# Performance work log

Hardware: AMD Instinct MI355X
Metric: run time of the kernel (lower is better)

## Reference

```python
import jax, jax.numpy as jnp
from jax import lax
import numpy as np

B, IN, HID, OUT, E = 32768, 512, 1024, 2, 64
N_MEM, N_ITER = 100, 10


def setup_inputs() -> dict:
    key = jax.random.key(0)
    ks = jax.random.split(key, 10)
    x = jax.random.normal(ks[0], (B, IN), dtype=jnp.float32)
    # encoder params (Linear stored as [in, out] for x @ W + b)
    e_w1 = jax.random.normal(ks[1], (IN, HID), dtype=jnp.float32) * 0.02
    e_b1 = jnp.zeros((HID,), dtype=jnp.float32)
    e_w2 = jax.random.normal(ks[2], (HID, E), dtype=jnp.float32) * 0.02
    e_b2 = jnp.zeros((E,), dtype=jnp.float32)
    # Hopfield weights: sum of outer products of N_MEM bipolar memories, zero diag, /N_MEM
    mems = jnp.where(jax.random.bernoulli(ks[3], 0.5, (N_MEM, E)), 1.0, -1.0)
    hop_w = (mems.T @ mems) / N_MEM
    hop_w = hop_w * (1.0 - jnp.eye(E, dtype=jnp.float32))
    # Q-network params
    n_w1 = jax.random.normal(ks[4], (IN + E, HID), dtype=jnp.float32) * 0.02
    n_b1 = jnp.zeros((HID,), dtype=jnp.float32)
    n_w2 = jax.random.normal(ks[5], (HID, HID), dtype=jnp.float32) * 0.02
    n_b2 = jnp.zeros((HID,), dtype=jnp.float32)
    n_w3 = jax.random.normal(ks[6], (HID, OUT), dtype=jnp.float32) * 0.02
    n_b3 = jnp.zeros((OUT,), dtype=jnp.float32)
    return {"x": x, "e_w1": e_w1, "e_b1": e_b1, "e_w2": e_w2, "e_b2": e_b2,
            "hop_w": hop_w, "n_w1": n_w1, "n_b1": n_b1, "n_w2": n_w2,
            "n_b2": n_b2, "n_w3": n_w3, "n_b3": n_b3}


def _retrieve(probe, hop_w):
    # Asynchronous Hopfield retrieval, batched over B.
    # probe: [B, E]; state in {+1,-1}
    state = jnp.where(probe > 0, 1.0, -1.0)
    idxs = jnp.arange(E)

    def unit_step(state, xs):
        i, w_row = xs  # w_row: [E]
        act = state @ w_row  # [B]
        state = state.at[:, i].set(jnp.where(act > 0, 1.0, -1.0))
        return state, None

    def iter_body(state, _):
        state, _ = lax.scan(unit_step, state, (idxs, hop_w))
        return state, None

    state, _ = lax.scan(iter_body, state, None, length=N_ITER)
    return jnp.where(state > 0, 1.0, 0.0)


def reference(x, e_w1, e_b1, e_w2, e_b2, hop_w, n_w1, n_b1, n_w2, n_b2, n_w3, n_b3):
    encoded = jax.nn.relu(x @ e_w1 + e_b1) @ e_w2 + e_b2  # [B, E]
    retrieved = lax.stop_gradient(_retrieve(encoded, hop_w))  # detached in original
    combined = jnp.concatenate([x, retrieved], axis=1)  # [B, IN+E]
    h = jax.nn.relu(combined @ n_w1 + n_b1)
    h = jax.nn.relu(h @ n_w2 + n_b2)
    return h @ n_w3 + n_b3  # [B, OUT]
```

## Files before the change

kernel.cpp:

```cpp
#include <hip/hip_runtime.h>
#include <hip/hip_bf16.h>
#include <stdint.h>
#include <math.h>

typedef __attribute__((ext_vector_type(4))) float f32x4;
typedef __attribute__((ext_vector_type(8))) __bf16 bf16x8;
typedef __attribute__((ext_vector_type(8))) uint16_t u16x8;
typedef __attribute__((ext_vector_type(4))) uint32_t u32x4;

__device__ __forceinline__ uint16_t f2bf(float f) {
  union { float f; uint32_t u; } v; v.f = f;
  uint32_t r = v.u + 0x7FFFu + ((v.u >> 16) & 1u);
  return (uint16_t)(r >> 16);
}
__device__ __forceinline__ float bf2f(uint16_t b) {
  union { uint32_t u; float f; } v; v.u = ((uint32_t)b) << 16;
  return v.f;
}
__device__ __forceinline__ void gload16(const void* g, void* l) {
  __builtin_amdgcn_global_load_lds(
      (const __attribute__((address_space(1))) uint32_t*)g,
      (__attribute__((address_space(3))) uint32_t*)l, 16, 0, 0);
}

__global__ __launch_bounds__(256) void k_conv_x(const float* __restrict__ x,
                                                uint16_t* __restrict__ comb) {
  int i = blockIdx.x * 256 + threadIdx.x;
  int base = i * 8;
  int row = base >> 9;
  int col = base & 511;
  const float* src = x + base;
  f32x4 a = *(const f32x4*)src;
  f32x4 b = *(const f32x4*)(src + 4);
  u16x8 o;
  o[0] = f2bf(a[0]); o[1] = f2bf(a[1]); o[2] = f2bf(a[2]); o[3] = f2bf(a[3]);
  o[4] = f2bf(b[0]); o[5] = f2bf(b[1]); o[6] = f2bf(b[2]); o[7] = f2bf(b[3]);
  *(u16x8*)(comb + (size_t)row * 576 + col) = o;
}

__global__ __launch_bounds__(256) void k_convT(const float* __restrict__ W,
                                               uint16_t* __restrict__ WT,
                                               int K, int N) {
  __shared__ float tile[64][65];
  const int t = threadIdx.x;
  const int n0 = blockIdx.x * 64, k0 = blockIdx.y * 64;
  const int c = t & 63, r0 = t >> 6;
#pragma unroll
  for (int rr = 0; rr < 16; ++rr) {
    int r = r0 * 16 + rr;
    tile[r][c] = W[(size_t)(k0 + r) * N + n0 + c];
  }
  __syncthreads();
#pragma unroll
  for (int rr = 0; rr < 16; ++rr) {
    int r = r0 * 16 + rr;
    WT[(size_t)(n0 + r) * K + k0 + c] = f2bf(tile[c][r]);
  }
}

__global__ __launch_bounds__(256) void k_conv(const float* __restrict__ W,
                                              uint16_t* __restrict__ O, int n) {
  int i = blockIdx.x * 256 + threadIdx.x;
  if (i < n) O[i] = f2bf(W[i]);
}

template <int K, bool RELU>
__global__ __launch_bounds__(256, 4)
void k_enc(const float* __restrict__ A, const float* __restrict__ W,
           const float* __restrict__ bias, float* __restrict__ C, int N) {
  __shared__ __align__(16) float xs[32][128];
  __shared__ __align__(16) float ws[32][68];
  const int t = threadIdx.x;
  const int m0 = blockIdx.y * 128, n0 = blockIdx.x * 64;
  const int mg = t >> 4, ng = t & 15;

  float res[8][4], acc[8][4];
#pragma unroll
  for (int i = 0; i < 8; ++i)
#pragma unroll
    for (int j = 0; j < 4; ++j) { res[i][j] = 0.f; acc[i][j] = 0.f; }

  const int xr = t >> 1, xk = (t & 1) * 16;
  const int wrr = t >> 3, wj = (t & 7) * 8;

  for (int c = 0; c < K / 32; ++c) {
    const int k0 = c * 32;
    if (k0 > 0 && (k0 % 384) == 0) {
#pragma unroll
      for (int i = 0; i < 8; ++i)
#pragma unroll
        for (int j = 0; j < 4; ++j) { res[i][j] += acc[i][j]; acc[i][j] = 0.f; }
    }
    __syncthreads();
#pragma unroll
    for (int u = 0; u < 4; ++u) {
      f32x4 v = *(const f32x4*)(A + (size_t)(m0 + xr) * K + k0 + xk + u * 4);
      xs[xk + u * 4 + 0][xr] = v[0];
      xs[xk + u * 4 + 1][xr] = v[1];
      xs[xk + u * 4 + 2][xr] = v[2];
      xs[xk + u * 4 + 3][xr] = v[3];
    }
#pragma unroll
    for (int u = 0; u < 2; ++u)
      *(f32x4*)&ws[wrr][wj + u * 4] =
          *(const f32x4*)(W + (size_t)(k0 + wrr) * N + n0 + wj + u * 4);
    __syncthreads();
#pragma unroll
    for (int k = 0; k < 32; ++k) {
      f32x4 x0 = *(const f32x4*)&xs[k][mg * 8];
      f32x4 x1 = *(const f32x4*)&xs[k][mg * 8 + 4];
      f32x4 wv = *(const f32x4*)&ws[k][ng * 4];
#pragma unroll
      for (int j = 0; j < 4; ++j) {
        acc[0][j] = fmaf(x0[0], wv[j], acc[0][j]);
        acc[1][j] = fmaf(x0[1], wv[j], acc[1][j]);
        acc[2][j] = fmaf(x0[2], wv[j], acc[2][j]);
        acc[3][j] = fmaf(x0[3], wv[j], acc[3][j]);
        acc[4][j] = fmaf(x1[0], wv[j], acc[4][j]);
        acc[5][j] = fmaf(x1[1], wv[j], acc[5][j]);
        acc[6][j] = fmaf(x1[2], wv[j], acc[6][j]);
        acc[7][j] = fmaf(x1[3], wv[j], acc[7][j]);
      }
    }
  }
#pragma unroll
  for (int i = 0; i < 8; ++i)
#pragma unroll
    for (int j = 0; j < 4; ++j) res[i][j] += acc[i][j];

#pragma unroll
  for (int i = 0; i < 8; ++i) {
    f32x4 o;
#pragma unroll
    for (int j = 0; j < 4; ++j) {
      float v = res[i][j] + bias[n0 + ng * 4 + j];
      if (RELU) v = fmaxf(v, 0.f);
      o[j] = v;
    }
    *(f32x4*)(C + (size_t)(m0 + mg * 8 + i) * N + n0 + ng * 4) = o;
  }
}

#define KNIFE_TAU 1e-6f

__device__ __forceinline__ uint32_t retrieve_bits(uint32_t sm,
                                                  const float (*w)[64],
                                                  int l) {
  for (int it = 0; it < 10; ++it) {
    bool changed = false;
    for (int i = 0; i < 64; ++i) {
      float r = 0.f;
#pragma unroll
      for (int c = 0; c < 8; ++c) {
        float wv = w[i][8 * c + l];
        uint32_t flip = ((~sm >> c) & 1u) << 31;
        r += __uint_as_float(__float_as_uint(wv) ^ flip);
      }
      r += __shfl_xor(r, 1);
      r += __shfl_xor(r, 2);
      r += __shfl_xor(r, 4);
      uint32_t nb = r > 0.f ? 1u : 0u;
      if ((i & 7) == l) {
        uint32_t g = i >> 3;
        uint32_t ob = (sm >> g) & 1u;
        changed |= (nb != ob);
        sm = (sm & ~(1u << g)) | (nb << g);
      }
    }
    if (!__any(changed)) break;
  }
  return sm;
}

__device__ __forceinline__ uint64_t gather_mask_bits(uint32_t sm, int g) {
  uint64_t m = 0;
#pragma unroll
  for (int c = 0; c < 8; ++c) {
    unsigned long long b = __ballot(((sm >> c) & 1u) != 0u);
    m |= (uint64_t)((b >> (g * 8)) & 0xFFull) << (8 * c);
  }
  return m;
}

__global__ __launch_bounds__(256) void k_hopfield(const float* __restrict__ enc,
                                                  const float* __restrict__ hw,
                                                  uint16_t* __restrict__ comb) {
  __shared__ __align__(16) float w[64][64];
  const int t = threadIdx.x;
#pragma unroll
  for (int i = 0; i < 4; ++i)
    ((f32x4*)&w[0][0])[t * 4 + i] = ((const f32x4*)hw)[t * 4 + i];
  __syncthreads();

  const int lane = t & 63, wv = t >> 6;
  const int g = lane >> 3, l = lane & 7;
  const int sid = (blockIdx.x * 4 + wv) * 8 + g;
  const float* er = enc + (size_t)sid * 64;

  uint32_t imask = 0;
  int kc = -1;
  bool kpos = false;
#pragma unroll
  for (int c = 0; c < 8; ++c) {
    float v = er[8 * c + l];
    if (v > 0.f) imask |= (1u << c);
    if (kc < 0 && fabsf(v) < KNIFE_TAU) { kc = c; kpos = v > 0.f; }
  }
  unsigned long long kb = __ballot(kc >= 0);
  uint32_t gbits = (uint32_t)((kb >> (g * 8)) & 0xFFull);
  bool hasknife = gbits != 0;
  int klane = g * 8 + (__ffs(gbits) - 1);
  bool is_kl = hasknife && (lane == klane);
  uint32_t kbit = (kc >= 0) ? (1u << (kc & 7)) : 0u;

  uint32_t ma_bits = is_kl ? (imask | kbit) : imask;
  uint64_t mA = gather_mask_bits(retrieve_bits(ma_bits, w, l), g);
  uint64_t m = mA;

  if (__any(hasknife)) {
    if (hasknife) {
      uint32_t mb_bits = is_kl ? (imask & ~kbit) : imask;
      uint64_t mB = gather_mask_bits(retrieve_bits(mb_bits, w, l), g);
      if (mA != mB) {
        int kp = __shfl(kpos ? 1 : 0, klane);
        m = kp ? mA : mB;
      }
    }
  }

  uint32_t byte = (uint32_t)((m >> (8 * l)) & 0xFFull);
  u32x4 o;
#pragma unroll
  for (int p = 0; p < 4; ++p) {
    uint32_t lo = ((byte >> (2 * p)) & 1u) ? 0x3F80u : 0u;
    uint32_t hi = ((byte >> (2 * p + 1)) & 1u) ? 0x3F800000u : 0u;
    o[p] = lo | hi;
  }
  *(u32x4*)(comb + (size_t)sid * 576 + 512 + l * 8) = o;
}

__global__ __launch_bounds__(256)
void k_gemm_bf16(const uint16_t* __restrict__ A, const uint16_t* __restrict__ BT,
                 const float* __restrict__ bias, uint16_t* __restrict__ C,
                 int M, int N, int K, int relu) {
  constexpr int BM = 128, BN = 128, BK = 32;
  __shared__ __align__(16) uint16_t As[BM][BK];
  __shared__ __align__(16) uint16_t Bs[BN][BK];
  const int t = threadIdx.x;
  const int lane = t & 63, wid = t >> 6;
  const int wr = wid >> 1, wc = wid & 1;
  const int bm = blockIdx.y * BM, bn = blockIdx.x * BN;

  f32x4 acc[4][4] = {};

  const int l15 = lane & 15, kb = (lane >> 4) * 8;
  const int i0 = t, i1 = t + 256;
  const int r0 = i0 >> 2, c0 = (i0 & 3) * 8;
  const int r1 = i1 >> 2, c1 = (i1 & 3) * 8;
  const uint16_t* A0 = A + (size_t)(bm + r0) * K + c0;
  const uint16_t* A1 = A + (size_t)(bm + r1) * K + c1;
  const uint16_t* B0 = BT + (size_t)(bn + r0) * K + c0;
  const uint16_t* B1 = BT + (size_t)(bn + r1) * K + c1;
  uint16_t* Al = &As[0][0];
  uint16_t* Bl = &Bs[0][0];

  for (int kt = 0; kt < K / BK; ++kt) {
    __syncthreads();
    const int ko = kt * BK;
    gload16(A0 + ko, Al + i0 * 8);
    gload16(A1 + ko, Al + i1 * 8);
    gload16(B0 + ko, Bl + i0 * 8);
    gload16(B1 + ko, Bl + i1 * 8);
    __syncthreads();
    bf16x8 af[4], bf[4];
#pragma unroll
    for (int m = 0; m < 4; ++m)
      af[m] = *(const bf16x8*)&As[wr * 64 + m * 16 + l15][kb];
#pragma unroll
    for (int n = 0; n < 4; ++n)
      bf[n] = *(const bf16x8*)&Bs[wc * 64 + n * 16 + l15][kb];
#pragma unroll
    for (int m = 0; m < 4; ++m)
#pragma unroll
      for (int n = 0; n < 4; ++n)
        acc[m][n] = __builtin_amdgcn_mfma_f32_16x16x32_bf16(af[m], bf[n],
                                                            acc[m][n], 0, 0, 0);
  }
#pragma unroll
  for (int m = 0; m < 4; ++m) {
    int row = bm + wr * 64 + m * 16 + (lane >> 4) * 4;
#pragma unroll
    for (int n = 0; n < 4; ++n) {
      int col = bn + wc * 64 + n * 16 + l15;
      float bsv = bias[col];
#pragma unroll
      for (int r = 0; r < 4; ++r) {
        float v = acc[m][n][r] + bsv;
        if (relu) v = fmaxf(v, 0.f);
        C[(size_t)(row + r) * N + col] = f2bf(v);
      }
    }
  }
}

__global__ __launch_bounds__(256) void k_n3(const uint16_t* __restrict__ h2,
                                            const uint16_t* __restrict__ w3,
                                            const float* __restrict__ b3,
                                            float* __restrict__ out, int M) {
  const int lane = threadIdx.x & 63;
  const int wglob = (blockIdx.x * 256 + threadIdx.x) >> 6;
  const int nw = (gridDim.x * 256) >> 6;
  u16x8 wa = *(const u16x8*)(w3 + lane * 16);
  u16x8 wb = *(const u16x8*)(w3 + lane * 16 + 8);
  u16x8 wc = *(const u16x8*)(w3 + 1024 + lane * 16);
  u16x8 wd = *(const u16x8*)(w3 + 1024 + lane * 16 + 8);
  const float b0 = b3[0], b1 = b3[1];
  for (int row = wglob; row < M; row += nw) {
    const uint16_t* hr = h2 + (size_t)row * 1024;
    u16x8 h0 = *(const u16x8*)(hr + lane * 8);
    u16x8 h1 = *(const u16x8*)(hr + 512 + lane * 8);
    float a0 = 0.f, a1 = 0.f;
#pragma unroll
    for (int e = 0; e < 4; ++e) {
      float h = bf2f(h0[e]);
      a0 = fmaf(h, bf2f(wa[2 * e]), a0);
      a1 = fmaf(h, bf2f(wa[2 * e + 1]), a1);
    }
#pragma unroll
    for (int e = 4; e < 8; ++e) {
      float h = bf2f(h0[e]);
      a0 = fmaf(h, bf2f(wb[2 * e - 8]), a0);
      a1 = fmaf(h, bf2f(wb[2 * e - 7]), a1);
    }
#pragma unroll
    for (int e = 0; e < 4; ++e) {
      float h = bf2f(h1[e]);
      a0 = fmaf(h, bf2f(wc[2 * e]), a0);
      a1 = fmaf(h, bf2f(wc[2 * e + 1]), a1);
    }
#pragma unroll
    for (int e = 4; e < 8; ++e) {
      float h = bf2f(h1[e]);
      a0 = fmaf(h, bf2f(wd[2 * e - 8]), a0);
      a1 = fmaf(h, bf2f(wd[2 * e - 7]), a1);
    }
#pragma unroll
    for (int off = 32; off; off >>= 1) {
      a0 += __shfl_xor(a0, off, 64);
      a1 += __shfl_xor(a1, off, 64);
    }
    if (lane == 0) {
      out[(size_t)row * 2 + 0] = a0 + b0;
      out[(size_t)row * 2 + 1] = a1 + b1;
    }
  }
}

extern "C" void kernel_launch(void* const* d_in, const int* in_sizes, int n_in,
                              void* d_out, int out_size, void* d_ws, size_t ws_size,
                              hipStream_t stream) {
  const float* x     = (const float*)d_in[0];
  const float* e_w1  = (const float*)d_in[1];
  const float* e_b1  = (const float*)d_in[2];
  const float* e_w2  = (const float*)d_in[3];
  const float* e_b2  = (const float*)d_in[4];
  const float* hop_w = (const float*)d_in[5];
  const float* n_w1  = (const float*)d_in[6];
  const float* n_b1  = (const float*)d_in[7];
  const float* n_w2  = (const float*)d_in[8];
  const float* n_b2  = (const float*)d_in[9];
  const float* n_w3  = (const float*)d_in[10];
  const float* n_b3  = (const float*)d_in[11];
  float* out = (float*)d_out;
  char* ws = (char*)d_ws;

  float*    h1e  = (float*)(ws + 0);
  uint16_t* h1   = (uint16_t*)(ws + 0);
  uint16_t* h2   = (uint16_t*)(ws + 67108864);
  uint16_t* comb = (uint16_t*)(ws + 134217728);
  float*    enc  = (float*)(ws + 171966464);
  uint16_t* w1t  = (uint16_t*)(ws + 180355072);
  uint16_t* w2t  = (uint16_t*)(ws + 181534720);
  uint16_t* w3b  = (uint16_t*)(ws + 183631872);

  k_conv_x<<<8192, 256, 0, stream>>>(x, comb);
  k_convT<<<dim3(1024 / 64, 576 / 64), 256, 0, stream>>>(n_w1, w1t, 576, 1024);
  k_convT<<<dim3(1024 / 64, 1024 / 64), 256, 0, stream>>>(n_w2, w2t, 1024, 1024);
  k_conv<<<(2048 + 255) / 256, 256, 0, stream>>>(n_w3, w3b, 2048);

  k_enc<512, true><<<dim3(1024 / 64, 32768 / 128), 256, 0, stream>>>(
      x, e_w1, e_b1, h1e, 1024);
  k_enc<1024, false><<<dim3(1, 32768 / 128), 256, 0, stream>>>(
      h1e, e_w2, e_b2, enc, 64);

  k_hopfield<<<32768 / 32, 256, 0, stream>>>(enc, hop_w, comb);

  k_gemm_bf16<<<dim3(1024 / 128, 32768 / 128), 256, 0, stream>>>(
      comb, w1t, n_b1, h1, 32768, 1024, 576, 1);
  k_gemm_bf16<<<dim3(1024 / 128, 32768 / 128), 256, 0, stream>>>(
      h1, w2t, n_b2, h2, 32768, 1024, 1024, 1);
  k_n3<<<512, 256, 0, stream>>>(h2, w3b, n_b3, out, 32768);
}
```

Before: 980.4 us.

## Add small-tile encoder kernel, remap GEMM blocks for XCD locality, raise occupancy

Replaces the second encoder GEMM (N=64), which previously ran only 256 blocks, with a new kernel using 32-row tiles so 1024 blocks fill the GPU. It also remaps GEMM block indices so consecutive blocks land on the same XCD, sharing weight and activation tiles in L2. It raises the launch-bounds occupancy hint for the first encoder kernel, which may cause register spilling.

```diff
diff --git a/kernel.cpp b/kernel.cpp
--- a/kernel.cpp
+++ b/kernel.cpp
@@ -65,7 +65,7 @@
 }
 
 template <int K, bool RELU>
-__global__ __launch_bounds__(256, 4)
+__global__ __launch_bounds__(256, 6)
 void k_enc(const float* __restrict__ A, const float* __restrict__ W,
            const float* __restrict__ bias, float* __restrict__ C, int N) {
   __shared__ __align__(16) float xs[32][128];
@@ -138,6 +138,66 @@
       o[j] = v;
     }
     *(f32x4*)(C + (size_t)(m0 + mg * 8 + i) * N + n0 + ng * 4) = o;
+  }
+}
+
+__global__ __launch_bounds__(256, 8)
+void k_enc2(const float* __restrict__ A, const float* __restrict__ W,
+            const float* __restrict__ bias, float* __restrict__ C) {
+  __shared__ __align__(16) float xs[32][36];
+  __shared__ __align__(16) float ws[32][68];
+  const int t = threadIdx.x;
+  const int m0 = blockIdx.x * 32;
+  const int mg = t >> 4, ng = t & 15;
+
+  float res[2][4] = {}, acc[2][4] = {};
+  const int xr = t >> 3, xk4 = (t & 7) * 4;
+  const int wrr = t >> 3, wj = (t & 7) * 8;
+
+  for (int c = 0; c < 32; ++c) {
+    const int k0 = c * 32;
+    if (k0 > 0 && (k0 % 384) == 0) {
+#pragma unroll
+      for (int i = 0; i < 2; ++i)
+#pragma unroll
+        for (int j = 0; j < 4; ++j) { res[i][j] += acc[i][j]; acc[i][j] = 0.f; }
+    }
+    __syncthreads();
+    {
+      f32x4 v = *(const f32x4*)(A + (size_t)(m0 + xr) * 1024 + k0 + xk4);
+      xs[xk4 + 0][xr] = v[0];
+      xs[xk4 + 1][xr] = v[1];
+      xs[xk4 + 2][xr] = v[2];
+      xs[xk4 + 3][xr] = v[3];
+    }
+#pragma unroll
+    for (int u = 0; u < 2; ++u)
+      *(f32x4*)&ws[wrr][wj + u * 4] =
+          *(const f32x4*)(W + (size_t)(k0 + wrr) * 64 + wj + u * 4);
+    __syncthreads();
+#pragma unroll
+    for (int k = 0; k < 32; ++k) {
+      float x0 = xs[k][mg * 2 + 0];
+      float x1 = xs[k][mg * 2 + 1];
+      f32x4 wv = *(const f32x4*)&ws[k][ng * 4];
+#pragma unroll
+      for (int j = 0; j < 4; ++j) {
+        acc[0][j] = fmaf(x0, wv[j], acc[0][j]);
+        acc[1][j] = fmaf(x1, wv[j], acc[1][j]);
+      }
+    }
+  }
+#pragma unroll
+  for (int i = 0; i < 2; ++i)
+#pragma unroll
+    for (int j = 0; j < 4; ++j) res[i][j] += acc[i][j];
+
+#pragma unroll
+  for (int i = 0; i < 2; ++i) {
+    f32x4 o;
+#pragma unroll
+    for (int j = 0; j < 4; ++j) o[j] = res[i][j] + bias[ng * 4 + j];
+    *(f32x4*)(C + (size_t)(m0 + mg * 2 + i) * 64 + ng * 4) = o;
   }
 }
 
@@ -249,7 +309,16 @@
   const int t = threadIdx.x;
   const int lane = t & 63, wid = t >> 6;
   const int wr = wid >> 1, wc = wid & 1;
-  const int bm = blockIdx.y * BM, bn = blockIdx.x * BN;
+
+  int bxi = blockIdx.x, byi = blockIdx.y;
+  if ((gridDim.x & 7) == 0) {
+    int L = byi * gridDim.x + bxi;
+    int cpx = (gridDim.x * gridDim.y) >> 3;
+    int T = (L & 7) * cpx + (L >> 3);
+    byi = T / gridDim.x;
+    bxi = T % gridDim.x;
+  }
+  const int bm = byi * BM, bn = bxi * BN;
 
   f32x4 acc[4][4] = {};
 
@@ -390,8 +459,7 @@
 
   k_enc<512, true><<<dim3(1024 / 64, 32768 / 128), 256, 0, stream>>>(
       x, e_w1, e_b1, h1e, 1024);
-  k_enc<1024, false><<<dim3(1, 32768 / 128), 256, 0, stream>>>(
-      h1e, e_w2, e_b2, enc, 64);
+  k_enc2<<<1024, 256, 0, stream>>>(h1e, e_w2, e_b2, enc);
 
   k_hopfield<<<32768 / 32, 256, 0, stream>>>(enc, hop_w, comb);
 
```

After: 1.043 ms. 1.06x slower.
